# Kernel tuning notes

Measured on AMD Instinct MI355X. Metric: run time of the kernel, lower is better.

The kernel has to match this reference:

```python
import jax, jax.numpy as jnp
import numpy as np


def _bitlinear(x, w_latent):
    # per-output-row abs-mean scale, ternary round with straight-through estimator
    scale = jax.lax.stop_gradient(
        jnp.clip(jnp.mean(jnp.abs(w_latent), axis=1, keepdims=True), 1e-5, None))
    tern = jnp.clip(jnp.round(w_latent / scale), -1.0, 1.0)
    w = w_latent + jax.lax.stop_gradient(tern - w_latent)  # STE
    return x @ (w * scale).T


def setup_inputs() -> dict:
    key = jax.random.key(0)
    ks = jax.random.split(key, 6)
    dim, hidden, rank = 1024, 4096, 16
    B, S = 4, 4096
    x = jax.random.normal(ks[0], (B, S, dim), dtype=jnp.float32)
    w_fc = 0.02 * jax.random.normal(ks[1], (hidden, dim), dtype=jnp.float32)
    w_proj = 0.02 * jax.random.normal(ks[2], (dim, hidden), dtype=jnp.float32)
    u = 0.02 * jax.random.normal(ks[3], (hidden, rank), dtype=jnp.float32)
    v = 0.02 * jax.random.normal(ks[4], (rank, dim), dtype=jnp.float32)
    fast_b = jax.random.normal(ks[5], (rank, rank), dtype=jnp.float32)
    gate = jnp.float32(0.05)
    return {"x": x, "fast_b": fast_b, "w_fc": w_fc, "w_proj": w_proj,
            "u": u, "v": v, "gate": gate}


def reference(x, fast_b, w_fc, w_proj, u, v, gate):
    # fc BitLinear + low-rank fast adapter delta
    h = _bitlinear(x, w_fc) + gate * (((x @ v.T) @ fast_b.T) @ u.T)
    r = jnp.maximum(h, 0.0)
    return _bitlinear(r * r, w_proj)  # ReLU^2 then proj BitLinear
```

## Files before the change

kernel.cpp:

```cpp
#include <hip/hip_runtime.h>


typedef unsigned short u16;
typedef __attribute__((ext_vector_type(8))) short short8;
typedef __attribute__((ext_vector_type(4))) float float4v;

#define M_TOK   16384
#define DIM     1024
#define HID     4096


__device__ __forceinline__ u16 f2bf(float f) {
    union { float f; unsigned u; } v; v.f = f;
    unsigned r = v.u + 0x7fffu + ((v.u >> 16) & 1u);
    return (u16)(r >> 16);
}

__device__ __forceinline__ void gload_lds16(const u16* g, u16* l) {
    __builtin_amdgcn_global_load_lds(
        (const __attribute__((address_space(1))) void*)g,
        (__attribute__((address_space(3))) void*)l, 16, 0, 0);
}


__global__ __launch_bounds__(256) void cvt_x_kernel(const float* __restrict__ x,
                                                    u16* __restrict__ y) {
    int i = (blockIdx.x * 256 + threadIdx.x) * 4;
    float4 v = *reinterpret_cast<const float4*>(x + i);
    ushort4 o;
    o.x = f2bf(v.x); o.y = f2bf(v.y); o.z = f2bf(v.z); o.w = f2bf(v.w);
    *reinterpret_cast<ushort4*>(y + i) = o;
}

__global__ __launch_bounds__(256) void adapter_T_kernel(const float* __restrict__ u,
                                                        const float* __restrict__ fb,
                                                        float* __restrict__ T) {
    int i = blockIdx.x * 256 + threadIdx.x;
    int row = i >> 4, r = i & 15;
    float s = 0.f;
#pragma unroll
    for (int k = 0; k < 16; k++) s += u[row * 16 + k] * fb[k * 16 + r];
    T[i] = s;
}

__global__ __launch_bounds__(256) void build_w1_kernel(const float* __restrict__ w,
                                                       const float* __restrict__ T,
                                                       const float* __restrict__ v,
                                                       const float* __restrict__ gate,
                                                       u16* __restrict__ W1) {
    const int row = blockIdx.x, tid = threadIdx.x;
    float s = 0.f;
#pragma unroll
    for (int jj = 0; jj < 4; jj++) s += fabsf(w[row * 1024 + tid + jj * 256]);
#pragma unroll
    for (int o = 32; o > 0; o >>= 1) s += __shfl_down(s, o, 64);
    __shared__ float red[4];
    if ((tid & 63) == 0) red[tid >> 6] = s;
    __syncthreads();
    const float scale = fmaxf((red[0] + red[1] + red[2] + red[3]) * (1.f / 1024.f), 1e-5f);
    const float g = gate[0];
    float t[16];
#pragma unroll
    for (int r = 0; r < 16; r++) t[r] = T[row * 16 + r];
#pragma unroll
    for (int jj = 0; jj < 4; jj++) {
        const int j = tid + jj * 256;
        const float wv = w[row * 1024 + j];
        float tern = rintf(wv / scale);
        tern = fminf(1.f, fmaxf(-1.f, tern));
        float ad = 0.f;
#pragma unroll
        for (int r = 0; r < 16; r++) ad += t[r] * v[r * 1024 + j];
        W1[row * 1024 + j] = f2bf(tern * scale + g * ad);
    }
}

__global__ __launch_bounds__(256) void build_w2_kernel(const float* __restrict__ w,
                                                       u16* __restrict__ W2) {
    const int row = blockIdx.x, tid = threadIdx.x;
    float s = 0.f;
#pragma unroll
    for (int jj = 0; jj < 16; jj++) s += fabsf(w[row * 4096 + tid + jj * 256]);
#pragma unroll
    for (int o = 32; o > 0; o >>= 1) s += __shfl_down(s, o, 64);
    __shared__ float red[4];
    if ((tid & 63) == 0) red[tid >> 6] = s;
    __syncthreads();
    const float scale = fmaxf((red[0] + red[1] + red[2] + red[3]) * (1.f / 4096.f), 1e-5f);
#pragma unroll
    for (int jj = 0; jj < 16; jj++) {
        const int j = tid + jj * 256;
        float tern = rintf(w[row * 4096 + j] / scale);
        tern = fminf(1.f, fmaxf(-1.f, tern));
        W2[row * 4096 + j] = f2bf(tern * scale);
    }
}

template <int N, int K, int EPI>
__global__ __launch_bounds__(512, 2) void gemm256(const u16* __restrict__ A,
                                                  const u16* __restrict__ B,
                                                  void* __restrict__ Cv) {
    constexpr int GM  = M_TOK / 256;
    constexpr int GN  = N / 256;
    constexpr int NWG = GM * GN;
    constexpr int NT  = K / 64;

    __shared__ alignas(16) u16 lds[2][2][256 * 64];

    const int tid  = threadIdx.x;
    const int wave = tid >> 6, lane = tid & 63;
    const int lr = lane & 15, quad = lane >> 4;
    const int wm = (wave >> 2) << 7;
    const int wn = (wave & 3) << 6;

    int flat = (int)blockIdx.x;
    flat = (flat & 7) * (NWG / 8) + (flat >> 3);
    const int bm = flat % GM;
    const int bn = flat / GM;

    const u16* Ag[4]; const u16* Bg[4]; int qo[4];
#pragma unroll
    for (int c = 0; c < 4; c++) {
        const int q = tid + c * 512;
        const int row = q >> 3, p = q & 7;
        const int kc = p ^ (row & 7);
        Ag[c] = A + (size_t)(bm * 256 + row) * K + kc * 8;
        Bg[c] = B + (size_t)(bn * 256 + row) * K + kc * 8;
        qo[c] = q * 8;
    }

    float4v acc[8][4];
#pragma unroll
    for (int i = 0; i < 8; i++)
#pragma unroll
        for (int j = 0; j < 4; j++) acc[i][j] = (float4v)0.0f;

    const int pk0 = (quad ^ (lr & 7)) * 8;
    const int pk1 = ((4 + quad) ^ (lr & 7)) * 8;

#define STAGE(buf, k0)                                                        \
    do {                                                                      \
        u16* la_ = &lds[buf][0][0]; u16* lb_ = &lds[buf][1][0];               \
        _Pragma("unroll")                                                     \
        for (int c_ = 0; c_ < 4; c_++) gload_lds16(Ag[c_] + (k0), la_ + qo[c_]); \
        _Pragma("unroll")                                                     \
        for (int c_ = 0; c_ < 4; c_++) gload_lds16(Bg[c_] + (k0), lb_ + qo[c_]); \
    } while (0)

#define BAR()                                                                 \
    do {                                                                      \
        __builtin_amdgcn_sched_barrier(0);                                    \
        __builtin_amdgcn_s_barrier();                                         \
        __builtin_amdgcn_sched_barrier(0);                                    \
    } while (0)

    STAGE(0, 0);
    STAGE(1, 64);
    __builtin_amdgcn_sched_barrier(0);
    asm volatile("s_waitcnt vmcnt(8)" ::: "memory");
    __builtin_amdgcn_s_barrier();
    __builtin_amdgcn_sched_barrier(0);
    asm volatile("" ::: "memory");

    for (int t = 0; t < NT; ++t) {
        const int cur = t & 1;
        const u16* Ab = &lds[cur][0][0];
        const u16* Bb = &lds[cur][1][0];
        short8 af[4][2], b0[2][2], b1[2][2];

#pragma unroll
        for (int i = 0; i < 4; i++) {
            const u16* rp = Ab + (wm + i * 16 + lr) * 64;
            af[i][0] = *reinterpret_cast<const short8*>(rp + pk0);
            af[i][1] = *reinterpret_cast<const short8*>(rp + pk1);
        }
#pragma unroll
        for (int j = 0; j < 2; j++) {
            const u16* rp = Bb + (wn + j * 16 + lr) * 64;
            b0[j][0] = *reinterpret_cast<const short8*>(rp + pk0);
            b0[j][1] = *reinterpret_cast<const short8*>(rp + pk1);
        }
        BAR();
        __builtin_amdgcn_s_setprio(1);
#pragma unroll
        for (int i = 0; i < 4; i++)
#pragma unroll
            for (int j = 0; j < 2; j++)
#pragma unroll
                for (int ks = 0; ks < 2; ks++)
                    acc[i][j] = __builtin_amdgcn_mfma_f32_16x16x32_bf16(
                        af[i][ks], b0[j][ks], acc[i][j], 0, 0, 0);
        __builtin_amdgcn_s_setprio(0);
        BAR();

#pragma unroll
        for (int j = 0; j < 2; j++) {
            const u16* rp = Bb + (wn + 32 + j * 16 + lr) * 64;
            b1[j][0] = *reinterpret_cast<const short8*>(rp + pk0);
            b1[j][1] = *reinterpret_cast<const short8*>(rp + pk1);
        }
        BAR();
        __builtin_amdgcn_s_setprio(1);
#pragma unroll
        for (int i = 0; i < 4; i++)
#pragma unroll
            for (int j = 0; j < 2; j++)
#pragma unroll
                for (int ks = 0; ks < 2; ks++)
                    acc[i][2 + j] = __builtin_amdgcn_mfma_f32_16x16x32_bf16(
                        af[i][ks], b1[j][ks], acc[i][2 + j], 0, 0, 0);
        __builtin_amdgcn_s_setprio(0);
        BAR();

#pragma unroll
        for (int i = 0; i < 4; i++) {
            const u16* rp = Ab + (wm + 64 + i * 16 + lr) * 64;
            af[i][0] = *reinterpret_cast<const short8*>(rp + pk0);
            af[i][1] = *reinterpret_cast<const short8*>(rp + pk1);
        }
        BAR();
        __builtin_amdgcn_s_setprio(1);
#pragma unroll
        for (int i = 0; i < 4; i++)
#pragma unroll
            for (int j = 0; j < 2; j++)
#pragma unroll
                for (int ks = 0; ks < 2; ks++)
                    acc[4 + i][j] = __builtin_amdgcn_mfma_f32_16x16x32_bf16(
                        af[i][ks], b0[j][ks], acc[4 + i][j], 0, 0, 0);
        __builtin_amdgcn_s_setprio(0);
        BAR();

        asm volatile("" ::: "memory");
        if (t + 2 < NT) {
            STAGE(cur, (t + 2) * 64);
        }
        __builtin_amdgcn_sched_barrier(0);
        __builtin_amdgcn_s_setprio(1);
#pragma unroll
        for (int i = 0; i < 4; i++)
#pragma unroll
            for (int j = 0; j < 2; j++)
#pragma unroll
                for (int ks = 0; ks < 2; ks++)
                    acc[4 + i][2 + j] = __builtin_amdgcn_mfma_f32_16x16x32_bf16(
                        af[i][ks], b1[j][ks], acc[4 + i][2 + j], 0, 0, 0);
        __builtin_amdgcn_s_setprio(0);
        __builtin_amdgcn_sched_barrier(0);
        if (t + 1 < NT) {
            if (t + 2 < NT) {
                asm volatile("s_waitcnt vmcnt(8)" ::: "memory");
            } else {
                asm volatile("s_waitcnt vmcnt(0)" ::: "memory");
            }
            __builtin_amdgcn_s_barrier();
            __builtin_amdgcn_sched_barrier(0);
            asm volatile("" ::: "memory");
        }
    }
#undef STAGE
#undef BAR

    const int row0 = bm * 256 + wm + quad * 4;
    const int col0 = bn * 256 + wn + lr;
#pragma unroll
    for (int qr = 0; qr < 2; qr++)
#pragma unroll
        for (int i = 0; i < 4; i++)
#pragma unroll
            for (int qc = 0; qc < 2; qc++)
#pragma unroll
                for (int j = 0; j < 2; j++) {
                    const int col = col0 + qc * 32 + j * 16;
                    const float4v a = acc[qr * 4 + i][qc * 2 + j];
#pragma unroll
                    for (int r = 0; r < 4; r++) {
                        const int row = row0 + qr * 64 + i * 16 + r;
                        if (EPI == 0) {
                            const float rr = fmaxf(a[r], 0.f);
                            ((u16*)Cv)[(size_t)row * N + col] = f2bf(rr * rr);
                        } else {
                            ((float*)Cv)[(size_t)row * N + col] = a[r];
                        }
                    }
                }
}


extern "C" void kernel_launch(void* const* d_in, const int* in_sizes, int n_in,
                              void* d_out, int out_size, void* d_ws, size_t ws_size,
                              hipStream_t stream) {
    const float* x      = (const float*)d_in[0];
    const float* fast_b = (const float*)d_in[1];
    const float* w_fc   = (const float*)d_in[2];
    const float* w_proj = (const float*)d_in[3];
    const float* u      = (const float*)d_in[4];
    const float* v      = (const float*)d_in[5];
    const float* gate   = (const float*)d_in[6];
    float* out = (float*)d_out;

    char* ws = (char*)d_ws;
    u16*   Xb  = (u16*)(ws + 0);
    u16*   W1  = (u16*)(ws + 33554432);
    u16*   W2  = (u16*)(ws + 41943040);
    u16*   RSQ = (u16*)(ws + 50331648);
    float* T   = (float*)(ws + 184549376);

    cvt_x_kernel<<<M_TOK * DIM / (256 * 4), 256, 0, stream>>>(x, Xb);
    adapter_T_kernel<<<HID * 16 / 256, 256, 0, stream>>>(u, fast_b, T);
    build_w1_kernel<<<HID, 256, 0, stream>>>(w_fc, T, v, gate, W1);
    build_w2_kernel<<<DIM, 256, 0, stream>>>(w_proj, W2);

    gemm256<HID, DIM, 0><<<dim3((M_TOK / 256) * (HID / 256)), 512, 0, stream>>>(Xb, W1, RSQ);
    gemm256<DIM, HID, 1><<<dim3((M_TOK / 256) * (DIM / 256)), 512, 0, stream>>>(RSQ, W2, out);
}
```

Baseline: 415.2 us.

## Fuse prologue kernels and software-pipeline LDS fragment loads in GEMM main loop

Merges the x conversion, adapter product, and both ternary weight builders into one block-indexed prologue launch, computing the small u·fast_b product inline per row. The GEMM main loop is restructured into eight 8-MFMA clusters, with the next fragment's LDS reads interleaved between clusters. It also drops the intermediate s_barriers between compute phases and prefetches the first fragments of the next K tile before the final cluster. This aims to cut launch overhead and hide LDS latency behind MFMA work, at the cost of more live registers, which could cause spills or reduce occupancy.

```diff
diff --git a/kernel.cpp b/kernel.cpp
--- a/kernel.cpp
+++ b/kernel.cpp
@@ -23,76 +23,69 @@
 }
 
 
-__global__ __launch_bounds__(256) void cvt_x_kernel(const float* __restrict__ x,
-                                                    u16* __restrict__ y) {
-    int i = (blockIdx.x * 256 + threadIdx.x) * 4;
-    float4 v = *reinterpret_cast<const float4*>(x + i);
-    ushort4 o;
-    o.x = f2bf(v.x); o.y = f2bf(v.y); o.z = f2bf(v.z); o.w = f2bf(v.w);
-    *reinterpret_cast<ushort4*>(y + i) = o;
-}
-
-__global__ __launch_bounds__(256) void adapter_T_kernel(const float* __restrict__ u,
-                                                        const float* __restrict__ fb,
-                                                        float* __restrict__ T) {
-    int i = blockIdx.x * 256 + threadIdx.x;
-    int row = i >> 4, r = i & 15;
-    float s = 0.f;
-#pragma unroll
-    for (int k = 0; k < 16; k++) s += u[row * 16 + k] * fb[k * 16 + r];
-    T[i] = s;
-}
-
-__global__ __launch_bounds__(256) void build_w1_kernel(const float* __restrict__ w,
-                                                       const float* __restrict__ T,
-                                                       const float* __restrict__ v,
-                                                       const float* __restrict__ gate,
-                                                       u16* __restrict__ W1) {
-    const int row = blockIdx.x, tid = threadIdx.x;
-    float s = 0.f;
-#pragma unroll
-    for (int jj = 0; jj < 4; jj++) s += fabsf(w[row * 1024 + tid + jj * 256]);
-#pragma unroll
-    for (int o = 32; o > 0; o >>= 1) s += __shfl_down(s, o, 64);
+__global__ __launch_bounds__(256) void prologue_kernel(
+    const float* __restrict__ x, const float* __restrict__ w_fc,
+    const float* __restrict__ w_proj, const float* __restrict__ u,
+    const float* __restrict__ fb, const float* __restrict__ v,
+    const float* __restrict__ gate,
+    u16* __restrict__ Xb, u16* __restrict__ W1, u16* __restrict__ W2) {
+    const int b = blockIdx.x, tid = threadIdx.x;
     __shared__ float red[4];
-    if ((tid & 63) == 0) red[tid >> 6] = s;
-    __syncthreads();
-    const float scale = fmaxf((red[0] + red[1] + red[2] + red[3]) * (1.f / 1024.f), 1e-5f);
-    const float g = gate[0];
-    float t[16];
-#pragma unroll
-    for (int r = 0; r < 16; r++) t[r] = T[row * 16 + r];
-#pragma unroll
-    for (int jj = 0; jj < 4; jj++) {
-        const int j = tid + jj * 256;
-        const float wv = w[row * 1024 + j];
-        float tern = rintf(wv / scale);
-        tern = fminf(1.f, fmaxf(-1.f, tern));
-        float ad = 0.f;
-#pragma unroll
-        for (int r = 0; r < 16; r++) ad += t[r] * v[r * 1024 + j];
-        W1[row * 1024 + j] = f2bf(tern * scale + g * ad);
-    }
-}
-
-__global__ __launch_bounds__(256) void build_w2_kernel(const float* __restrict__ w,
-                                                       u16* __restrict__ W2) {
-    const int row = blockIdx.x, tid = threadIdx.x;
-    float s = 0.f;
-#pragma unroll
-    for (int jj = 0; jj < 16; jj++) s += fabsf(w[row * 4096 + tid + jj * 256]);
-#pragma unroll
-    for (int o = 32; o > 0; o >>= 1) s += __shfl_down(s, o, 64);
-    __shared__ float red[4];
-    if ((tid & 63) == 0) red[tid >> 6] = s;
-    __syncthreads();
-    const float scale = fmaxf((red[0] + red[1] + red[2] + red[3]) * (1.f / 4096.f), 1e-5f);
-#pragma unroll
-    for (int jj = 0; jj < 16; jj++) {
-        const int j = tid + jj * 256;
-        float tern = rintf(w[row * 4096 + j] / scale);
-        tern = fminf(1.f, fmaxf(-1.f, tern));
-        W2[row * 4096 + j] = f2bf(tern * scale);
+
+    if (b < HID) {
+        const int row = b;
+        float s = 0.f;
+#pragma unroll
+        for (int jj = 0; jj < 4; jj++) s += fabsf(w_fc[row * 1024 + tid + jj * 256]);
+#pragma unroll
+        for (int o = 32; o > 0; o >>= 1) s += __shfl_down(s, o, 64);
+        if ((tid & 63) == 0) red[tid >> 6] = s;
+        __syncthreads();
+        const float scale = fmaxf((red[0] + red[1] + red[2] + red[3]) * (1.f / 1024.f), 1e-5f);
+        const float g = gate[0];
+        float t[16];
+#pragma unroll
+        for (int r = 0; r < 16; r++) t[r] = 0.f;
+#pragma unroll
+        for (int k = 0; k < 16; k++) {
+            const float uk = u[row * 16 + k];
+#pragma unroll
+            for (int r = 0; r < 16; r++) t[r] += uk * fb[k * 16 + r];
+        }
+#pragma unroll
+        for (int jj = 0; jj < 4; jj++) {
+            const int j = tid + jj * 256;
+            const float wv = w_fc[row * 1024 + j];
+            float tern = rintf(wv / scale);
+            tern = fminf(1.f, fmaxf(-1.f, tern));
+            float ad = 0.f;
+#pragma unroll
+            for (int r = 0; r < 16; r++) ad += t[r] * v[r * 1024 + j];
+            W1[row * 1024 + j] = f2bf(tern * scale + g * ad);
+        }
+    } else if (b < HID + DIM) {
+        const int row = b - HID;
+        float s = 0.f;
+#pragma unroll
+        for (int jj = 0; jj < 16; jj++) s += fabsf(w_proj[row * 4096 + tid + jj * 256]);
+#pragma unroll
+        for (int o = 32; o > 0; o >>= 1) s += __shfl_down(s, o, 64);
+        if ((tid & 63) == 0) red[tid >> 6] = s;
+        __syncthreads();
+        const float scale = fmaxf((red[0] + red[1] + red[2] + red[3]) * (1.f / 4096.f), 1e-5f);
+#pragma unroll
+        for (int jj = 0; jj < 16; jj++) {
+            const int j = tid + jj * 256;
+            float tern = rintf(w_proj[row * 4096 + j] / scale);
+            tern = fminf(1.f, fmaxf(-1.f, tern));
+            W2[row * 4096 + j] = f2bf(tern * scale);
+        }
+    } else {
+        const int i = (b - (HID + DIM)) * 1024 + tid * 4;
+        float4 vv = *reinterpret_cast<const float4*>(x + i);
+        ushort4 o;
+        o.x = f2bf(vv.x); o.y = f2bf(vv.y); o.z = f2bf(vv.z); o.w = f2bf(vv.w);
+        *reinterpret_cast<ushort4*>(Xb + i) = o;
     }
 }
 
@@ -137,6 +130,8 @@
 
     const int pk0 = (quad ^ (lr & 7)) * 8;
     const int pk1 = ((4 + quad) ^ (lr & 7)) * 8;
+    const int aoff = (wm + lr) * 64;
+    const int boff = (wn + lr) * 64;
 
 #define STAGE(buf, k0)                                                        \
     do {                                                                      \
@@ -147,119 +142,97 @@
         for (int c_ = 0; c_ < 4; c_++) gload_lds16(Bg[c_] + (k0), lb_ + qo[c_]); \
     } while (0)
 
-#define BAR()                                                                 \
+#define SB() __builtin_amdgcn_sched_barrier(0)
+
+#define CLUSTER8(ri, cj, Af, Bf)                                              \
     do {                                                                      \
-        __builtin_amdgcn_sched_barrier(0);                                    \
-        __builtin_amdgcn_s_barrier();                                         \
-        __builtin_amdgcn_sched_barrier(0);                                    \
+        SB();                                                                 \
+        __builtin_amdgcn_s_setprio(1);                                        \
+        _Pragma("unroll")                                                     \
+        for (int i_ = 0; i_ < 4; i_++) {                                      \
+            acc[(ri) + i_][(cj) + 0] = __builtin_amdgcn_mfma_f32_16x16x32_bf16( \
+                Af[i_], Bf[0], acc[(ri) + i_][(cj) + 0], 0, 0, 0);            \
+            acc[(ri) + i_][(cj) + 1] = __builtin_amdgcn_mfma_f32_16x16x32_bf16( \
+                Af[i_], Bf[1], acc[(ri) + i_][(cj) + 1], 0, 0, 0);            \
+        }                                                                     \
+        __builtin_amdgcn_s_setprio(0);                                        \
+        SB();                                                                 \
     } while (0)
+
+    short8 A0[4], A1[4], B0v[2], B1v[2];
+    short8 C0[4], C1[4], D0v[2], D1v[2];
 
     STAGE(0, 0);
     STAGE(1, 64);
-    __builtin_amdgcn_sched_barrier(0);
+    SB();
     asm volatile("s_waitcnt vmcnt(8)" ::: "memory");
     __builtin_amdgcn_s_barrier();
-    __builtin_amdgcn_sched_barrier(0);
-    asm volatile("" ::: "memory");
+    SB();
+    {
+        const u16* Ab = &lds[0][0][0]; const u16* Bb = &lds[0][1][0];
+#pragma unroll
+        for (int i = 0; i < 4; i++) A0[i]  = *reinterpret_cast<const short8*>(Ab + aoff + 1024 * i + pk0);
+#pragma unroll
+        for (int j = 0; j < 2; j++) B0v[j] = *reinterpret_cast<const short8*>(Bb + boff + 1024 * j + pk0);
+    }
 
     for (int t = 0; t < NT; ++t) {
-        const int cur = t & 1;
+        const int cur = t & 1, nxt = cur ^ 1;
         const u16* Ab = &lds[cur][0][0];
         const u16* Bb = &lds[cur][1][0];
-        short8 af[4][2], b0[2][2], b1[2][2];
-
-#pragma unroll
-        for (int i = 0; i < 4; i++) {
-            const u16* rp = Ab + (wm + i * 16 + lr) * 64;
-            af[i][0] = *reinterpret_cast<const short8*>(rp + pk0);
-            af[i][1] = *reinterpret_cast<const short8*>(rp + pk1);
-        }
-#pragma unroll
-        for (int j = 0; j < 2; j++) {
-            const u16* rp = Bb + (wn + j * 16 + lr) * 64;
-            b0[j][0] = *reinterpret_cast<const short8*>(rp + pk0);
-            b0[j][1] = *reinterpret_cast<const short8*>(rp + pk1);
-        }
-        BAR();
-        __builtin_amdgcn_s_setprio(1);
-#pragma unroll
-        for (int i = 0; i < 4; i++)
-#pragma unroll
-            for (int j = 0; j < 2; j++)
-#pragma unroll
-                for (int ks = 0; ks < 2; ks++)
-                    acc[i][j] = __builtin_amdgcn_mfma_f32_16x16x32_bf16(
-                        af[i][ks], b0[j][ks], acc[i][j], 0, 0, 0);
-        __builtin_amdgcn_s_setprio(0);
-        BAR();
-
-#pragma unroll
-        for (int j = 0; j < 2; j++) {
-            const u16* rp = Bb + (wn + 32 + j * 16 + lr) * 64;
-            b1[j][0] = *reinterpret_cast<const short8*>(rp + pk0);
-            b1[j][1] = *reinterpret_cast<const short8*>(rp + pk1);
-        }
-        BAR();
-        __builtin_amdgcn_s_setprio(1);
-#pragma unroll
-        for (int i = 0; i < 4; i++)
-#pragma unroll
-            for (int j = 0; j < 2; j++)
-#pragma unroll
-                for (int ks = 0; ks < 2; ks++)
-                    acc[i][2 + j] = __builtin_amdgcn_mfma_f32_16x16x32_bf16(
-                        af[i][ks], b1[j][ks], acc[i][2 + j], 0, 0, 0);
-        __builtin_amdgcn_s_setprio(0);
-        BAR();
-
-#pragma unroll
-        for (int i = 0; i < 4; i++) {
-            const u16* rp = Ab + (wm + 64 + i * 16 + lr) * 64;
-            af[i][0] = *reinterpret_cast<const short8*>(rp + pk0);
-            af[i][1] = *reinterpret_cast<const short8*>(rp + pk1);
-        }
-        BAR();
-        __builtin_amdgcn_s_setprio(1);
-#pragma unroll
-        for (int i = 0; i < 4; i++)
-#pragma unroll
-            for (int j = 0; j < 2; j++)
-#pragma unroll
-                for (int ks = 0; ks < 2; ks++)
-                    acc[4 + i][j] = __builtin_amdgcn_mfma_f32_16x16x32_bf16(
-                        af[i][ks], b0[j][ks], acc[4 + i][j], 0, 0, 0);
-        __builtin_amdgcn_s_setprio(0);
-        BAR();
-
-        asm volatile("" ::: "memory");
-        if (t + 2 < NT) {
-            STAGE(cur, (t + 2) * 64);
-        }
-        __builtin_amdgcn_sched_barrier(0);
-        __builtin_amdgcn_s_setprio(1);
-#pragma unroll
-        for (int i = 0; i < 4; i++)
-#pragma unroll
-            for (int j = 0; j < 2; j++)
-#pragma unroll
-                for (int ks = 0; ks < 2; ks++)
-                    acc[4 + i][2 + j] = __builtin_amdgcn_mfma_f32_16x16x32_bf16(
-                        af[i][ks], b1[j][ks], acc[4 + i][2 + j], 0, 0, 0);
-        __builtin_amdgcn_s_setprio(0);
-        __builtin_amdgcn_sched_barrier(0);
+
+#pragma unroll
+        for (int j = 0; j < 2; j++) B1v[j] = *reinterpret_cast<const short8*>(Bb + boff + 2048 + 1024 * j + pk0);
+        CLUSTER8(0, 0, A0, B0v);
+
+#pragma unroll
+        for (int i = 0; i < 4; i++) A1[i] = *reinterpret_cast<const short8*>(Ab + aoff + 4096 + 1024 * i + pk0);
+        CLUSTER8(0, 2, A0, B1v);
+
+#pragma unroll
+        for (int i = 0; i < 4; i++) C0[i] = *reinterpret_cast<const short8*>(Ab + aoff + 1024 * i + pk1);
+        CLUSTER8(4, 0, A1, B0v);
+
+#pragma unroll
+        for (int j = 0; j < 2; j++) D0v[j] = *reinterpret_cast<const short8*>(Bb + boff + 1024 * j + pk1);
+        CLUSTER8(4, 2, A1, B1v);
+
+#pragma unroll
+        for (int j = 0; j < 2; j++) D1v[j] = *reinterpret_cast<const short8*>(Bb + boff + 2048 + 1024 * j + pk1);
+        CLUSTER8(0, 0, C0, D0v);
+
+#pragma unroll
+        for (int i = 0; i < 4; i++) C1[i] = *reinterpret_cast<const short8*>(Ab + aoff + 4096 + 1024 * i + pk1);
+        CLUSTER8(0, 2, C0, D1v);
+
+        CLUSTER8(4, 0, C1, D0v);
+
+        SB();
+        __builtin_amdgcn_s_barrier();
+        SB();
+        if (t + 2 < NT) STAGE(cur, (t + 2) * 64);
+        SB();
         if (t + 1 < NT) {
             if (t + 2 < NT) {
                 asm volatile("s_waitcnt vmcnt(8)" ::: "memory");
             } else {
                 asm volatile("s_waitcnt vmcnt(0)" ::: "memory");
             }
+            SB();
             __builtin_amdgcn_s_barrier();
-            __builtin_amdgcn_sched_barrier(0);
-            asm volatile("" ::: "memory");
-        }
+            SB();
+            const u16* An = &lds[nxt][0][0]; const u16* Bn = &lds[nxt][1][0];
+#pragma unroll
+            for (int i = 0; i < 4; i++) A0[i]  = *reinterpret_cast<const short8*>(An + aoff + 1024 * i + pk0);
+#pragma unroll
+            for (int j = 0; j < 2; j++) B0v[j] = *reinterpret_cast<const short8*>(Bn + boff + 1024 * j + pk0);
+        }
+
+        CLUSTER8(4, 2, C1, D1v);
     }
 #undef STAGE
-#undef BAR
+#undef SB
+#undef CLUSTER8
 
     const int row0 = bm * 256 + wm + quad * 4;
     const int col0 = bn * 256 + wn + lr;
@@ -304,12 +277,9 @@
     u16*   W1  = (u16*)(ws + 33554432);
     u16*   W2  = (u16*)(ws + 41943040);
     u16*   RSQ = (u16*)(ws + 50331648);
-    float* T   = (float*)(ws + 184549376);
-
-    cvt_x_kernel<<<M_TOK * DIM / (256 * 4), 256, 0, stream>>>(x, Xb);
-    adapter_T_kernel<<<HID * 16 / 256, 256, 0, stream>>>(u, fast_b, T);
-    build_w1_kernel<<<HID, 256, 0, stream>>>(w_fc, T, v, gate, W1);
-    build_w2_kernel<<<DIM, 256, 0, stream>>>(w_proj, W2);
+
+    prologue_kernel<<<HID + DIM + M_TOK * DIM / (256 * 4), 256, 0, stream>>>(
+        x, w_fc, w_proj, u, fast_b, v, gate, Xb, W1, W2);
 
     gemm256<HID, DIM, 0><<<dim3((M_TOK / 256) * (HID / 256)), 512, 0, stream>>>(Xb, W1, RSQ);
     gemm256<DIM, HID, 1><<<dim3((M_TOK / 256) * (DIM / 256)), 512, 0, stream>>>(RSQ, W2, out);
```

Result: faster. 395.2 us (-4.8%).
